# Optimization experiments

Measured on AMD Instinct MI355X. Metric: run time of the kernel, lower is better.

The kernel has to match this reference:

```python
import jax, jax.numpy as jnp
import numpy as np

K = 2048  # num_embeddings
D = 64    # embedding_dim


def setup_inputs() -> dict:
    key = jax.random.key(0)
    k1, k2 = jax.random.split(key)
    inputs = jax.random.normal(k1, (64, 32, 32, D), dtype=jnp.float32)
    # tf.random_uniform_initializer default: U[0, 1)
    embeddings = jax.random.uniform(k2, (K, D), dtype=jnp.float32)
    return {"inputs": inputs, "embeddings": embeddings}


def reference(inputs, embeddings):
    input_shape = inputs.shape
    flat_inputs = inputs.reshape(-1, D)  # [N, D]
    distances = (
        jnp.sum(flat_inputs ** 2, axis=1, keepdims=True)
        - 2.0 * jnp.matmul(flat_inputs, embeddings.T)
        + jnp.sum(embeddings ** 2, axis=1)
    )
    encoding_indices = jnp.argmin(distances, axis=1)  # [N]
    quantized = embeddings[encoding_indices].reshape(input_shape)
    # straight-through estimator
    quantized = inputs + jax.lax.stop_gradient(quantized - inputs)
    return quantized, encoding_indices, flat_inputs
```

## Files before the change

kernel.cpp:

```cpp
#include <hip/hip_runtime.h>
#include <cfloat>

#define N_TOTAL 65536
#define DIM     64
#define NEMB    2048

typedef __attribute__((ext_vector_type(8))) _Float16 half8;
typedef __attribute__((ext_vector_type(4))) float    floatx4;

__global__ void prep_kernel(const float* __restrict__ emb,
                            half8* __restrict__ ehp, float* __restrict__ en) {
    const int t = blockIdx.x * 256 + threadIdx.x;
    {
        const int l   = t & 63;
        const int ks  = (t >> 6) & 1;
        const int g   = t >> 7;
        const int col = g * 16 + (l & 15);
        const int kb  = ks * 32 + (l >> 4) * 8;
        const float* s = emb + col * DIM + kb;
        float4 v0 = *(const float4*)s, v1 = *(const float4*)(s + 4);
        half8 hv;
        hv[0] = (_Float16)v0.x; hv[1] = (_Float16)v0.y;
        hv[2] = (_Float16)v0.z; hv[3] = (_Float16)v0.w;
        hv[4] = (_Float16)v1.x; hv[5] = (_Float16)v1.y;
        hv[6] = (_Float16)v1.z; hv[7] = (_Float16)v1.w;
        ehp[t] = hv;
    }
    if (t < NEMB * 4) {
        const int row = t >> 2, seg = t & 3;
        const float* s = emb + row * DIM + seg * 16;
        float acc = 0.f;
#pragma unroll
        for (int i = 0; i < 4; ++i) {
            float4 v = ((const float4*)s)[i];
            acc = fmaf(v.x, v.x, acc); acc = fmaf(v.y, v.y, acc);
            acc = fmaf(v.z, v.z, acc); acc = fmaf(v.w, v.w, acc);
        }
        acc += __shfl_xor(acc, 1, 64);
        acc += __shfl_xor(acc, 2, 64);
        if (seg == 0) en[row] = acc;
    }
}

__global__ __launch_bounds__(256, 8) void vq_mfma_kernel(
        const float* __restrict__ x, const float* __restrict__ emb,
        const char* __restrict__ ehb, const float* __restrict__ eng,
        float* __restrict__ quant, float* __restrict__ idxf,
        float* __restrict__ flat) {

    __shared__ uint4 Mrg[2][32];

    const int t    = threadIdx.x;
    const int wave = t >> 6, lane = t & 63;
    const int n = lane & 15, q = lane >> 4;
    const int h = wave & 1, p = wave >> 1;
    const int blk0 = blockIdx.x * 32;
    const int row0 = blk0 + p * 16;

    {
        const float4* s4 = (const float4*)(x + (size_t)blk0 * DIM);
        float4*       d4 = (float4*)(flat + (size_t)blk0 * DIM);
#pragma unroll
        for (int i = 0; i < 2; ++i) d4[i * 256 + t] = s4[i * 256 + t];
    }

    half8 ah[2], al[2];
#pragma unroll
    for (int ks = 0; ks < 2; ++ks) {
        const float* pp = x + (size_t)(row0 + n) * DIM + ks * 32 + q * 8;
        float4 v0 = *(const float4*)pp, v1 = *(const float4*)(pp + 4);
        float xv[8] = {v0.x, v0.y, v0.z, v0.w, v1.x, v1.y, v1.z, v1.w};
#pragma unroll
        for (int j = 0; j < 8; ++j) {
            _Float16 hh = (_Float16)xv[j];
            ah[ks][j] = hh;
            al[ks][j] = (_Float16)(xv[j] - (float)hh);
        }
    }

    unsigned maskv;
    asm("v_mov_b32 %0, 0xFFFFFFC0" : "=v"(maskv));

    unsigned best[4], sec[4];
#pragma unroll
    for (int r = 0; r < 4; ++r) { best[r] = 0u; sec[r] = 0u; }

    const char*  ebase = ehb + (size_t)h * 131072 + (size_t)lane * 16;
    const float* enp   = eng + h * 1024 + n;

    half8 sbuf[2][2];
    float enc[2];
#pragma unroll
    for (int j = 0; j < 2; ++j) {
        const char* src = ebase + (size_t)j * 2048;
        sbuf[j][0] = *(const half8*)(src);
        sbuf[j][1] = *(const half8*)(src + 1024);
        enc[j]     = enp[j * 16];
    }

#pragma unroll 2
    for (int i = 0; i < 64; ++i) {
        const int buf = i & 1;

        const float enh = fmaf(-0.5f, enc[buf], 128.0f);
        floatx4 e4 = {enh, enh, enh, enh};
        __builtin_amdgcn_s_setprio(1);
        floatx4 a0 = __builtin_amdgcn_mfma_f32_16x16x32_f16(ah[0], sbuf[buf][0], e4, 0, 0, 0);
        a0 = __builtin_amdgcn_mfma_f32_16x16x32_f16(al[0], sbuf[buf][0], a0, 0, 0, 0);
        a0 = __builtin_amdgcn_mfma_f32_16x16x32_f16(ah[1], sbuf[buf][1], a0, 0, 0, 0);
        a0 = __builtin_amdgcn_mfma_f32_16x16x32_f16(al[1], sbuf[buf][1], a0, 0, 0, 0);
        __builtin_amdgcn_s_setprio(0);

        if (i < 62) {
            const char* src = ebase + (size_t)(i + 2) * 2048;
            sbuf[buf][0] = *(const half8*)(src);
            sbuf[buf][1] = *(const half8*)(src + 1024);
            enc[buf]     = enp[(i + 2) * 16];
        }

        const unsigned Lp = (unsigned)(63 - i);
#pragma unroll
        for (int r = 0; r < 4; ++r) {
            unsigned key = (__float_as_uint(a0[r]) & maskv) | Lp;
            unsigned nb  = best[r] > key ? best[r] : key;
            unsigned ns;
            asm("v_med3_u32 %0, %1, %2, %3"
                : "=v"(ns) : "v"(best[r]), "v"(sec[r]), "v"(key));
            sec[r]  = ns;
            best[r] = nb;
        }
    }

    unsigned bval[4], bcol[4], sval[4], scol[4];
#pragma unroll
    for (int r = 0; r < 4; ++r) {
        bval[r] = best[r] & 0xFFFFFFC0u;
        bcol[r] = (unsigned)(h * 1024 + (63 - (int)(best[r] & 63u)) * 16 + n);
        sval[r] = sec[r] & 0xFFFFFFC0u;
        scol[r] = (unsigned)(h * 1024 + (63 - (int)(sec[r] & 63u)) * 16 + n);
    }
#pragma unroll
    for (int m = 1; m < 16; m <<= 1) {
#pragma unroll
        for (int r = 0; r < 4; ++r) {
            unsigned ov  = (unsigned)__shfl_xor((int)bval[r], m, 64);
            unsigned oc  = (unsigned)__shfl_xor((int)bcol[r], m, 64);
            unsigned ov2 = (unsigned)__shfl_xor((int)sval[r], m, 64);
            unsigned oc2 = (unsigned)__shfl_xor((int)scol[r], m, 64);
            bool ow = (ov > bval[r]) || (ov == bval[r] && oc < bcol[r]);
            unsigned nbv = ow ? ov : bval[r], nbc = ow ? oc : bcol[r];
            unsigned lv  = ow ? bval[r] : ov, lc  = ow ? bcol[r] : oc;
            bool sv2 = (ov2 > sval[r]) || (ov2 == sval[r] && oc2 < scol[r]);
            unsigned bsv = sv2 ? ov2 : sval[r], bsc = sv2 ? oc2 : scol[r];
            bool s3 = (lv > bsv) || (lv == bsv && lc < bsc);
            sval[r] = s3 ? lv : bsv; scol[r] = s3 ? lc : bsc;
            bval[r] = nbv; bcol[r] = nbc;
        }
    }
    if (n == 0) {
#pragma unroll
        for (int r = 0; r < 4; ++r) {
            const int lr = p * 16 + q * 4 + r;
            Mrg[h][lr] = make_uint4(bval[r], bcol[r], sval[r], scol[r]);
        }
    }
    __syncthreads();

#pragma unroll
    for (int rr = 0; rr < 2; ++rr) {
        const int lr   = wave * 8 + q * 2 + rr;
        const int grow = blk0 + lr;
        uint4 c0v = Mrg[0][lr], c1v = Mrg[1][lr];
        int cand[4] = {(int)c0v.y, (int)c0v.w, (int)c1v.y, (int)c1v.w};
        float4 xv = *(const float4*)(x + (size_t)grow * DIM + n * 4);
        float pbest = -FLT_MAX; int cbest = 0;
        float4 ebest = {0.f, 0.f, 0.f, 0.f};
#pragma unroll
        for (int c = 0; c < 4; ++c) {
            float4 e = *(const float4*)(emb + (size_t)cand[c] * DIM + n * 4);
            float pp = (xv.x - 0.5f * e.x) * e.x + (xv.y - 0.5f * e.y) * e.y
                     + (xv.z - 0.5f * e.z) * e.z + (xv.w - 0.5f * e.w) * e.w;
#pragma unroll
            for (int m2 = 1; m2 < 16; m2 <<= 1) pp += __shfl_xor(pp, m2, 64);
            bool take = (pp > pbest) || (pp == pbest && cand[c] < cbest);
            pbest = take ? pp : pbest;
            cbest = take ? cand[c] : cbest;
            ebest.x = take ? e.x : ebest.x; ebest.y = take ? e.y : ebest.y;
            ebest.z = take ? e.z : ebest.z; ebest.w = take ? e.w : ebest.w;
        }
        *(float4*)(quant + (size_t)grow * DIM + n * 4) = ebest;
        if (n == 0) idxf[grow] = (float)cbest;
    }
}

extern "C" void kernel_launch(void* const* d_in, const int* in_sizes, int n_in,
                              void* d_out, int out_size, void* d_ws, size_t ws_size,
                              hipStream_t stream) {
    const float* x   = (const float*)d_in[0];
    const float* emb = (const float*)d_in[1];
    float* out   = (float*)d_out;
    float* quant = out;
    float* idxf  = out + (size_t)N_TOTAL * DIM;
    float* flat  = idxf + N_TOTAL;

    half8* ehp = (half8*)d_ws;
    float* en  = (float*)((char*)d_ws + (size_t)NEMB * DIM * 2);

    prep_kernel<<<64, 256, 0, stream>>>(emb, ehp, en);
    vq_mfma_kernel<<<N_TOTAL / 32, 256, 0, stream>>>(x, emb, (const char*)ehp, en,
                                                     quant, idxf, flat);
}
```

Measured before the change: 125.2 us.

## Tile 64 rows per block with per-wave codebook quarters and drop fp16 split

```diff
diff --git a/kernel.cpp b/kernel.cpp
--- a/kernel.cpp
+++ b/kernel.cpp
@@ -42,51 +42,48 @@
     }
 }
 
-__global__ __launch_bounds__(256, 8) void vq_mfma_kernel(
+__global__ __launch_bounds__(256, 4) void vq_mfma_kernel(
         const float* __restrict__ x, const float* __restrict__ emb,
         const char* __restrict__ ehb, const float* __restrict__ eng,
         float* __restrict__ quant, float* __restrict__ idxf,
         float* __restrict__ flat) {
 
-    __shared__ uint4 Mrg[2][32];
+    __shared__ uint4 Mrg[4][64];
 
     const int t    = threadIdx.x;
     const int wave = t >> 6, lane = t & 63;
     const int n = lane & 15, q = lane >> 4;
-    const int h = wave & 1, p = wave >> 1;
-    const int blk0 = blockIdx.x * 32;
-    const int row0 = blk0 + p * 16;
+    const int blk0 = blockIdx.x * 64;
 
     {
         const float4* s4 = (const float4*)(x + (size_t)blk0 * DIM);
         float4*       d4 = (float4*)(flat + (size_t)blk0 * DIM);
 #pragma unroll
-        for (int i = 0; i < 2; ++i) d4[i * 256 + t] = s4[i * 256 + t];
-    }
-
-    half8 ah[2], al[2];
-#pragma unroll
-    for (int ks = 0; ks < 2; ++ks) {
-        const float* pp = x + (size_t)(row0 + n) * DIM + ks * 32 + q * 8;
-        float4 v0 = *(const float4*)pp, v1 = *(const float4*)(pp + 4);
-        float xv[8] = {v0.x, v0.y, v0.z, v0.w, v1.x, v1.y, v1.z, v1.w};
-#pragma unroll
-        for (int j = 0; j < 8; ++j) {
-            _Float16 hh = (_Float16)xv[j];
-            ah[ks][j] = hh;
-            al[ks][j] = (_Float16)(xv[j] - (float)hh);
-        }
-    }
+        for (int i = 0; i < 4; ++i) d4[i * 256 + t] = s4[i * 256 + t];
+    }
+
+    half8 ah[4][2];
+#pragma unroll
+    for (int tl = 0; tl < 4; ++tl)
+#pragma unroll
+        for (int ks = 0; ks < 2; ++ks) {
+            const float* pp = x + (size_t)(blk0 + tl * 16 + n) * DIM + ks * 32 + q * 8;
+            float4 v0 = *(const float4*)pp, v1 = *(const float4*)(pp + 4);
+            float xv[8] = {v0.x, v0.y, v0.z, v0.w, v1.x, v1.y, v1.z, v1.w};
+#pragma unroll
+            for (int j = 0; j < 8; ++j)
+                ah[tl][ks][j] = (_Float16)xv[j];
+        }
 
     unsigned maskv;
     asm("v_mov_b32 %0, 0xFFFFFFC0" : "=v"(maskv));
 
-    unsigned best[4], sec[4];
-#pragma unroll
-    for (int r = 0; r < 4; ++r) { best[r] = 0u; sec[r] = 0u; }
-
-    const char*  ebase = ehb + (size_t)h * 131072 + (size_t)lane * 16;
-    const float* enp   = eng + h * 1024 + n;
+    unsigned best[16], sec[16];
+#pragma unroll
+    for (int r = 0; r < 16; ++r) { best[r] = 0u; sec[r] = 0u; }
+
+    const char*  ebase = ehb + (size_t)wave * 65536 + (size_t)lane * 16;
+    const float* enp   = eng + wave * 512 + n;
 
     half8 sbuf[2][2];
     float enc[2];
@@ -99,19 +96,25 @@
     }
 
 #pragma unroll 2
-    for (int i = 0; i < 64; ++i) {
+    for (int i = 0; i < 32; ++i) {
         const int buf = i & 1;
 
         const float enh = fmaf(-0.5f, enc[buf], 128.0f);
         floatx4 e4 = {enh, enh, enh, enh};
+        half8 bk0 = sbuf[buf][0];
+        half8 bk1 = sbuf[buf][1];
         __builtin_amdgcn_s_setprio(1);
-        floatx4 a0 = __builtin_amdgcn_mfma_f32_16x16x32_f16(ah[0], sbuf[buf][0], e4, 0, 0, 0);
-        a0 = __builtin_amdgcn_mfma_f32_16x16x32_f16(al[0], sbuf[buf][0], a0, 0, 0, 0);
-        a0 = __builtin_amdgcn_mfma_f32_16x16x32_f16(ah[1], sbuf[buf][1], a0, 0, 0, 0);
-        a0 = __builtin_amdgcn_mfma_f32_16x16x32_f16(al[1], sbuf[buf][1], a0, 0, 0, 0);
+        floatx4 a0 = __builtin_amdgcn_mfma_f32_16x16x32_f16(ah[0][0], bk0, e4, 0, 0, 0);
+        floatx4 a1 = __builtin_amdgcn_mfma_f32_16x16x32_f16(ah[1][0], bk0, e4, 0, 0, 0);
+        floatx4 a2 = __builtin_amdgcn_mfma_f32_16x16x32_f16(ah[2][0], bk0, e4, 0, 0, 0);
+        floatx4 a3 = __builtin_amdgcn_mfma_f32_16x16x32_f16(ah[3][0], bk0, e4, 0, 0, 0);
+        a0 = __builtin_amdgcn_mfma_f32_16x16x32_f16(ah[0][1], bk1, a0, 0, 0, 0);
+        a1 = __builtin_amdgcn_mfma_f32_16x16x32_f16(ah[1][1], bk1, a1, 0, 0, 0);
+        a2 = __builtin_amdgcn_mfma_f32_16x16x32_f16(ah[2][1], bk1, a2, 0, 0, 0);
+        a3 = __builtin_amdgcn_mfma_f32_16x16x32_f16(ah[3][1], bk1, a3, 0, 0, 0);
         __builtin_amdgcn_s_setprio(0);
 
-        if (i < 62) {
+        if (i < 30) {
             const char* src = ebase + (size_t)(i + 2) * 2048;
             sbuf[buf][0] = *(const half8*)(src);
             sbuf[buf][1] = *(const half8*)(src + 1024);
@@ -120,8 +123,10 @@
 
         const unsigned Lp = (unsigned)(63 - i);
 #pragma unroll
-        for (int r = 0; r < 4; ++r) {
-            unsigned key = (__float_as_uint(a0[r]) & maskv) | Lp;
+        for (int r = 0; r < 16; ++r) {
+            float v = (r < 4) ? a0[r] : (r < 8) ? a1[r - 4]
+                    : (r < 12) ? a2[r - 8] : a3[r - 12];
+            unsigned key = (__float_as_uint(v) & maskv) | Lp;
             unsigned nb  = best[r] > key ? best[r] : key;
             unsigned ns;
             asm("v_med3_u32 %0, %1, %2, %3"
@@ -131,18 +136,18 @@
         }
     }
 
-    unsigned bval[4], bcol[4], sval[4], scol[4];
-#pragma unroll
-    for (int r = 0; r < 4; ++r) {
+    unsigned bval[16], bcol[16], sval[16], scol[16];
+#pragma unroll
+    for (int r = 0; r < 16; ++r) {
         bval[r] = best[r] & 0xFFFFFFC0u;
-        bcol[r] = (unsigned)(h * 1024 + (63 - (int)(best[r] & 63u)) * 16 + n);
+        bcol[r] = (unsigned)(wave * 512 + (63 - (int)(best[r] & 63u)) * 16 + n);
         sval[r] = sec[r] & 0xFFFFFFC0u;
-        scol[r] = (unsigned)(h * 1024 + (63 - (int)(sec[r] & 63u)) * 16 + n);
+        scol[r] = (unsigned)(wave * 512 + (63 - (int)(sec[r] & 63u)) * 16 + n);
     }
 #pragma unroll
     for (int m = 1; m < 16; m <<= 1) {
 #pragma unroll
-        for (int r = 0; r < 4; ++r) {
+        for (int r = 0; r < 16; ++r) {
             unsigned ov  = (unsigned)__shfl_xor((int)bval[r], m, 64);
             unsigned oc  = (unsigned)__shfl_xor((int)bcol[r], m, 64);
             unsigned ov2 = (unsigned)__shfl_xor((int)sval[r], m, 64);
@@ -159,24 +164,28 @@
     }
     if (n == 0) {
 #pragma unroll
-        for (int r = 0; r < 4; ++r) {
-            const int lr = p * 16 + q * 4 + r;
-            Mrg[h][lr] = make_uint4(bval[r], bcol[r], sval[r], scol[r]);
+        for (int r = 0; r < 16; ++r) {
+            const int lr = (r >> 2) * 16 + q * 4 + (r & 3);
+            Mrg[wave][lr] = make_uint4(bval[r], bcol[r], sval[r], scol[r]);
         }
     }
     __syncthreads();
 
 #pragma unroll
-    for (int rr = 0; rr < 2; ++rr) {
-        const int lr   = wave * 8 + q * 2 + rr;
+    for (int rr = 0; rr < 4; ++rr) {
+        const int lr   = wave * 16 + q * 4 + rr;
         const int grow = blk0 + lr;
         uint4 c0v = Mrg[0][lr], c1v = Mrg[1][lr];
-        int cand[4] = {(int)c0v.y, (int)c0v.w, (int)c1v.y, (int)c1v.w};
+        uint4 c2v = Mrg[2][lr], c3v = Mrg[3][lr];
+        int cand[8] = {(int)(c0v.y & 2047u), (int)(c0v.w & 2047u),
+                       (int)(c1v.y & 2047u), (int)(c1v.w & 2047u),
+                       (int)(c2v.y & 2047u), (int)(c2v.w & 2047u),
+                       (int)(c3v.y & 2047u), (int)(c3v.w & 2047u)};
         float4 xv = *(const float4*)(x + (size_t)grow * DIM + n * 4);
         float pbest = -FLT_MAX; int cbest = 0;
         float4 ebest = {0.f, 0.f, 0.f, 0.f};
 #pragma unroll
-        for (int c = 0; c < 4; ++c) {
+        for (int c = 0; c < 8; ++c) {
             float4 e = *(const float4*)(emb + (size_t)cand[c] * DIM + n * 4);
             float pp = (xv.x - 0.5f * e.x) * e.x + (xv.y - 0.5f * e.y) * e.y
                      + (xv.z - 0.5f * e.z) * e.z + (xv.w - 0.5f * e.w) * e.w;
@@ -207,6 +216,6 @@
     float* en  = (float*)((char*)d_ws + (size_t)NEMB * DIM * 2);
 
     prep_kernel<<<64, 256, 0, stream>>>(emb, ehp, en);
-    vq_mfma_kernel<<<N_TOTAL / 32, 256, 0, stream>>>(x, emb, (const char*)ehp, en,
+    vq_mfma_kernel<<<N_TOTAL / 64, 256, 0, stream>>>(x, emb, (const char*)ehp, en,
                                                      quant, idxf, flat);
 }
```

Result: slower. 156.3 us (+24.8%).
